# Performance work log

Hardware: AMD Instinct MI355X
Metric: run time of the kernel (lower is better)

Reference implementation:

```python
import jax, jax.numpy as jnp
import numpy as np

S_LEN, BATCH, D, HK, M, L, VOCAB = 1024, 4, 1024, 1024, 4096, 6, 32000
EPS = 1e-5


def layernorm(x, g, b):
    mu = x.mean(-1, keepdims=True)
    xc = x - mu
    var = (xc * xc).mean(-1, keepdims=True)
    return xc * jax.lax.rsqrt(var + EPS) * g + b


def block(z, wq, wk, wv, wc, g1, bb1, w1, b1, w2, b2, g2, bb2):
    # Faithful to the torch block: permute (1,0,2) at entry, never permute back.
    x = jnp.swapaxes(z, 0, 1)  # [B', S', d]
    d = x.shape[-1]
    Q = jnp.einsum('bsd,ed->bse', x, wq)
    K = jnp.einsum('bsd,ed->bse', x, wk)
    V = jnp.einsum('bsd,ed->bse', x, wv)
    # NOTE: scale is sqrt(embed_dim)=sqrt(d), not sqrt(k); no causal mask (faithful).
    scores = jnp.einsum('bse,bte->bst', Q, K) / jnp.sqrt(jnp.asarray(d, x.dtype))
    A = jax.nn.softmax(scores, axis=-1)
    ctx = jnp.einsum('bst,bte->bse', A, V)
    att = jnp.einsum('bse,de->bsd', ctx, wc) + x
    h = layernorm(att, g1, bb1)
    # NOTE: no nonlinearity in the FFN (faithful to the source).
    f = jnp.einsum('bsd,md->bsm', h, w1) + b1
    f = jnp.einsum('bsm,dm->bsd', f, w2) + b2
    return layernorm(f + h, g2, bb2)


def forward(x, word_emb, pos_emb, wq, wk, wv, wc, ln1_g, ln1_b, w1, b1, w2, b2,
            ln2_g, ln2_b, dec_w, dec_b, out_bias):
    S = x.shape[0]
    z = word_emb[x] * jnp.sqrt(jnp.asarray(D, word_emb.dtype))  # [S,B,d]
    z = jax.nn.relu(z + pos_emb[jnp.arange(S)][:, None, :])
    for i in range(L):  # small fixed layer count; shapes alternate layout so no scan
        z = block(z, wq[i], wk[i], wv[i], wc[i], ln1_g[i], ln1_b[i],
                  w1[i], b1[i], w2[i], b2[i], ln2_g[i], ln2_b[i])
    logits = jnp.einsum('sbd,vd->sbv', z, dec_w) + dec_b + out_bias
    return jax.nn.log_softmax(logits, axis=-1)


def setup_inputs() -> dict:
    key = jax.random.key(0)
    ks = jax.random.split(key, 16)
    std = jnp.float32(0.02)
    return {
        'x': jax.random.randint(ks[0], (S_LEN, BATCH), 0, VOCAB),
        'word_emb': jax.random.normal(ks[1], (VOCAB, D), jnp.float32) * std,
        'pos_emb': jax.random.normal(ks[2], (S_LEN, D), jnp.float32) * std,
        'wq': jax.random.normal(ks[3], (L, HK, D), jnp.float32) * std,
        'wk': jax.random.normal(ks[4], (L, HK, D), jnp.float32) * std,
        'wv': jax.random.normal(ks[5], (L, HK, D), jnp.float32) * std,
        'wc': jax.random.normal(ks[6], (L, D, HK), jnp.float32) * std,
        'ln1_g': jnp.ones((L, D), jnp.float32),
        'ln1_b': jnp.zeros((L, D), jnp.float32),
        'w1': jax.random.normal(ks[7], (L, M, D), jnp.float32) * std,
        'b1': jnp.zeros((L, M), jnp.float32),
        'w2': jax.random.normal(ks[8], (L, D, M), jnp.float32) * std,
        'b2': jnp.zeros((L, D), jnp.float32),
        'ln2_g': jnp.ones((L, D), jnp.float32),
        'ln2_b': jnp.zeros((L, D), jnp.float32),
        'dec_w': jax.random.normal(ks[9], (VOCAB, D), jnp.float32) * std,
        'dec_b': jnp.zeros((VOCAB,), jnp.float32),
        'out_bias': jnp.zeros((VOCAB,), jnp.float32),
    }


def reference(x, word_emb, pos_emb, wq, wk, wv, wc, ln1_g, ln1_b, w1, b1, w2, b2,
              ln2_g, ln2_b, dec_w, dec_b, out_bias):
    return forward(x, word_emb, pos_emb, wq, wk, wv, wc, ln1_g, ln1_b, w1, b1,
                   w2, b2, ln2_g, ln2_b, dec_w, dec_b, out_bias)
```

## Files before the change

### kernel.cpp

```cpp
#include <hip/hip_runtime.h>

typedef short short8 __attribute__((ext_vector_type(8)));
typedef float f32x4 __attribute__((ext_vector_type(4)));

#define DMODEL 1024
#define HKDIM 1024
#define MDIM 4096
#define NROW 4096
#define VOCAB 32000
#define NLAYER 6

#define GLOAD_LDS16(g, l)                                                      \
  __builtin_amdgcn_global_load_lds(                                            \
      (const __attribute__((address_space(1))) void*)(g),                      \
      (__attribute__((address_space(3))) void*)(l), 16, 0, 0)

__device__ __forceinline__ unsigned short f2bf(float f) {
  unsigned u = __float_as_uint(f);
  u += 0x7fffu + ((u >> 16) & 1u);
  return (unsigned short)(u >> 16);
}
__device__ __forceinline__ float bf2f(unsigned short h) {
  return __uint_as_float(((unsigned)h) << 16);
}
__device__ __forceinline__ float wave_sum(float v) {
  for (int o = 32; o; o >>= 1) v += __shfl_xor(v, o);
  return v;
}
__device__ __forceinline__ float wave_max(float v) {
  for (int o = 32; o; o >>= 1) v = fmaxf(v, __shfl_xor(v, o));
  return v;
}

__global__ __launch_bounds__(256) void k_embed(const int* __restrict__ x,
    const float* __restrict__ wemb, const float* __restrict__ pemb,
    float* __restrict__ z) {
  int r = blockIdx.x;
  int s = r >> 2;
  int tok = x[r];
  float4 a = ((const float4*)(wemb + (long)tok * DMODEL))[threadIdx.x];
  float4 p = ((const float4*)(pemb + (long)s * DMODEL))[threadIdx.x];
  float4 o;
  o.x = fmaxf(a.x * 32.0f + p.x, 0.0f);
  o.y = fmaxf(a.y * 32.0f + p.y, 0.0f);
  o.z = fmaxf(a.z * 32.0f + p.z, 0.0f);
  o.w = fmaxf(a.w * 32.0f + p.w, 0.0f);
  ((float4*)(z + (long)r * DMODEL))[threadIdx.x] = o;
}

__global__ __launch_bounds__(256) void k_permute(const float* __restrict__ zin,
    float* __restrict__ xf, unsigned short* __restrict__ xb, int A0, int A1) {
  int r = blockIdx.x;
  int a1 = r / A0, a0 = r - a1 * A0;
  float4 v = ((const float4*)(zin + (long)(a0 * A1 + a1) * DMODEL))[threadIdx.x];
  ((float4*)(xf + (long)r * DMODEL))[threadIdx.x] = v;
  ushort4 o = make_ushort4(f2bf(v.x), f2bf(v.y), f2bf(v.z), f2bf(v.w));
  ((ushort4*)(xb + (long)r * DMODEL))[threadIdx.x] = o;
}

__global__ __launch_bounds__(256) void k_cvt(const float* __restrict__ in,
    unsigned short* __restrict__ out, int n4) {
  int i = blockIdx.x * 256 + threadIdx.x;
  int stride = gridDim.x * 256;
  for (; i < n4; i += stride) {
    float4 v = ((const float4*)in)[i];
    ((ushort4*)out)[i] = make_ushort4(f2bf(v.x), f2bf(v.y), f2bf(v.z), f2bf(v.w));
  }
}

__global__ __launch_bounds__(256) void k_gemm_bt(
    const unsigned short* __restrict__ A, const unsigned short* __restrict__ B,
    float* __restrict__ Cf, unsigned short* __restrict__ Cb,
    const float* __restrict__ bias, const float* __restrict__ res,
    int M, int N, int K, int lda, int ldb, int ldc,
    long aB, long bB, long cB, float scale) {
  __shared__ unsigned short As[128 * 64];
  __shared__ unsigned short Bs[128 * 64];
  const int tid = threadIdx.x;
  const int gx = gridDim.x, gy = gridDim.y;

  int nwg = gx * gy * gridDim.z;
  int flat = blockIdx.x + gx * (blockIdx.y + gy * blockIdx.z);
  int q8 = nwg >> 3, r8 = nwg & 7;
  int xcd = flat & 7, inner = flat >> 3;
  int wg = (xcd < r8 ? xcd * (q8 + 1) : r8 * (q8 + 1) + (xcd - r8) * q8) + inner;
  int ty = wg % gy;
  int rest = wg / gy;
  int tx = rest % gx;
  int tz = rest / gx;

  const unsigned short* Ab = A + (long)tz * aB;
  const unsigned short* Bb = B + (long)tz * bB;
  const int row0 = ty * 128, col0 = tx * 128;
  const int lane = tid & 63, w = tid >> 6;
  const int wm = w >> 1, wn = w & 1;
  const int fr = lane & 15, fg = lane >> 4, fr7 = fr & 7;
  const int lrow = lane >> 3;
  const int lcol = ((lane & 7) ^ lrow) * 8;

  const unsigned short* aSrc = Ab + (long)(row0 + w * 32 + lrow) * lda + lcol;
  const unsigned short* bSrc = Bb + (long)(col0 + w * 32 + lrow) * ldb + lcol;
  unsigned short* aDst = As + w * 32 * 64;
  unsigned short* bDst = Bs + w * 32 * 64;

  f32x4 acc[4][4];
#pragma unroll
  for (int i = 0; i < 4; ++i)
#pragma unroll
    for (int j = 0; j < 4; ++j)
#pragma unroll
      for (int qq = 0; qq < 4; ++qq) acc[i][j][qq] = 0.0f;

  for (int k0 = 0; k0 < K; k0 += 64) {
#pragma unroll
    for (int i = 0; i < 4; ++i) {
      GLOAD_LDS16(aSrc + (long)i * 8 * lda + k0, aDst + i * 512);
      GLOAD_LDS16(bSrc + (long)i * 8 * ldb + k0, bDst + i * 512);
    }
    __syncthreads();
#pragma unroll
    for (int kk = 0; kk < 64; kk += 32) {
      short8 af[4], bfr[4];
#pragma unroll
      for (int i = 0; i < 4; ++i) {
        af[i] = *(const short8*)(As + (wm * 64 + i * 16 + fr) * 64 +
                                 (((kk >> 3) + fg) ^ fr7) * 8);
        bfr[i] = *(const short8*)(Bs + (wn * 64 + i * 16 + fr) * 64 +
                                  (((kk >> 3) + fg) ^ fr7) * 8);
      }
#pragma unroll
      for (int i = 0; i < 4; ++i)
#pragma unroll
        for (int j = 0; j < 4; ++j)
          acc[i][j] = __builtin_amdgcn_mfma_f32_16x16x32_bf16(af[i], bfr[j], acc[i][j], 0, 0, 0);
    }
    __syncthreads();
  }

#pragma unroll
  for (int j = 0; j < 4; ++j) {
    int col = col0 + wn * 64 + j * 16 + fr;
    float bv = bias ? bias[col] : 0.0f;
#pragma unroll
    for (int i = 0; i < 4; ++i) {
#pragma unroll
      for (int qq = 0; qq < 4; ++qq) {
        int row = row0 + wm * 64 + i * 16 + fg * 4 + qq;
        long off = cB * tz + (long)row * ldc + col;
        float v = acc[i][j][qq] * scale + bv;
        if (res) v += res[off];
        if (Cf) Cf[off] = v;
        if (Cb) Cb[off] = f2bf(v);
      }
    }
  }
}

__global__ __launch_bounds__(512, 2) void k_gemm8(
    const unsigned short* __restrict__ A, const unsigned short* __restrict__ B,
    float* __restrict__ Cf, unsigned short* __restrict__ Cb,
    const float* __restrict__ bias, int M, int N, int K,
    int lda, int ldb, int ldc) {
  __shared__ unsigned short As[2][256 * 64];
  __shared__ unsigned short Bs[2][256 * 64];
  const int tid = threadIdx.x;
  const int gx = gridDim.x, gy = gridDim.y;
  int nwg = gx * gy;
  int flat = blockIdx.x + gx * blockIdx.y;
  int q8 = nwg >> 3, r8 = nwg & 7;
  int xcd = flat & 7, inner = flat >> 3;
  int wg = (xcd < r8 ? xcd * (q8 + 1) : r8 * (q8 + 1) + (xcd - r8) * q8) + inner;
  int ty = wg % gy, tx = wg / gy;

  const int row0 = ty * 256, col0 = tx * 256;
  const int lane = tid & 63, w = tid >> 6;
  const int wm = w >> 2, wn = w & 3;
  const int fr = lane & 15, fg = lane >> 4, fr7 = fr & 7;
  const int srow = lane >> 3;
  const int scol = ((lane & 7) ^ srow) * 8;

  const unsigned short* pA = A + (size_t)(row0 + w * 32 + srow) * lda + scol;
  const unsigned short* pB = B + (size_t)(col0 + w * 32 + srow) * ldb + scol;
  unsigned short* aD0 = &As[0][w * 32 * 64];
  unsigned short* bD0 = &Bs[0][w * 32 * 64];
  unsigned short* aD1 = &As[1][w * 32 * 64];
  unsigned short* bD1 = &Bs[1][w * 32 * 64];

  auto stage = [&](int bf, int tk) {
    unsigned short* aD = bf ? aD1 : aD0;
    unsigned short* bD = bf ? bD1 : bD0;
#pragma unroll
    for (int i = 0; i < 4; ++i) {
      GLOAD_LDS16(pA + (size_t)i * 8 * lda + (size_t)tk * 64, aD + i * 512);
      GLOAD_LDS16(pB + (size_t)i * 8 * ldb + (size_t)tk * 64, bD + i * 512);
    }
  };
  auto rdA = [&](const unsigned short* lds, int i, int kq) -> short8 {
    return *(const short8*)(lds + (wm * 128 + i * 16 + fr) * 64 +
                            (((kq << 2) + fg) ^ fr7) * 8);
  };
  auto rdB = [&](const unsigned short* lds, int j, int kq) -> short8 {
    return *(const short8*)(lds + (wn * 64 + j * 16 + fr) * 64 +
                            (((kq << 2) + fg) ^ fr7) * 8);
  };

  f32x4 acc[8][4];
#pragma unroll
  for (int i = 0; i < 8; ++i)
#pragma unroll
    for (int j = 0; j < 4; ++j)
#pragma unroll
      for (int qq = 0; qq < 4; ++qq) acc[i][j][qq] = 0.0f;

  const int NT = K >> 6;

  stage(0, 0);
  __syncthreads();

  for (int t = 0; t < NT; ++t) {
    const unsigned short* aL = (t & 1) ? &As[1][0] : &As[0][0];
    const unsigned short* bL = (t & 1) ? &Bs[1][0] : &Bs[0][0];
    if (t + 1 < NT) stage((t & 1) ^ 1, t + 1);
#pragma unroll
    for (int kq = 0; kq < 2; ++kq) {
      short8 a8[8], b8[4];
#pragma unroll
      for (int i = 0; i < 8; ++i) a8[i] = rdA(aL, i, kq);
#pragma unroll
      for (int j = 0; j < 4; ++j) b8[j] = rdB(bL, j, kq);
#pragma unroll
      for (int i = 0; i < 8; ++i)
#pragma unroll
        for (int j = 0; j < 4; ++j)
          acc[i][j] = __builtin_amdgcn_mfma_f32_16x16x32_bf16(a8[i], b8[j], acc[i][j], 0, 0, 0);
    }
    __syncthreads();
  }

#pragma unroll
  for (int j = 0; j < 4; ++j) {
    int col = col0 + wn * 64 + j * 16 + fr;
    float bv = bias ? bias[col] : 0.0f;
#pragma unroll
    for (int i = 0; i < 8; ++i) {
#pragma unroll
      for (int qq = 0; qq < 4; ++qq) {
        int row = row0 + wm * 128 + i * 16 + fg * 4 + qq;
        size_t off = (size_t)row * ldc + col;
        float v = acc[i][j][qq] + bv;
        if (Cf) Cf[off] = v;
        if (Cb) Cb[off] = f2bf(v);
      }
    }
  }
}

__global__ __launch_bounds__(256) void k_ln(const float* __restrict__ X,
    const float* __restrict__ X2, const float* __restrict__ g,
    const float* __restrict__ b, float* __restrict__ outF,
    unsigned short* __restrict__ outB) {
  __shared__ float sm[4];
  int row = blockIdx.x, t = threadIdx.x;
  float4 v = ((const float4*)(X + (long)row * DMODEL))[t];
  if (X2) {
    float4 u = ((const float4*)(X2 + (long)row * DMODEL))[t];
    v.x += u.x; v.y += u.y; v.z += u.z; v.w += u.w;
  }
  float s = wave_sum(v.x + v.y + v.z + v.w);
  if ((t & 63) == 0) sm[t >> 6] = s;
  __syncthreads();
  float mean = (sm[0] + sm[1] + sm[2] + sm[3]) * (1.0f / DMODEL);
  __syncthreads();
  float4 c;
  c.x = v.x - mean; c.y = v.y - mean; c.z = v.z - mean; c.w = v.w - mean;
  float ss = wave_sum(c.x * c.x + c.y * c.y + c.z * c.z + c.w * c.w);
  if ((t & 63) == 0) sm[t >> 6] = ss;
  __syncthreads();
  float var = (sm[0] + sm[1] + sm[2] + sm[3]) * (1.0f / DMODEL);
  float rs = rsqrtf(var + 1e-5f);
  float4 gv = ((const float4*)g)[t], bv = ((const float4*)b)[t];
  float4 o;
  o.x = c.x * rs * gv.x + bv.x;
  o.y = c.y * rs * gv.y + bv.y;
  o.z = c.z * rs * gv.z + bv.z;
  o.w = c.w * rs * gv.w + bv.w;
  if (outF) ((float4*)(outF + (long)row * DMODEL))[t] = o;
  if (outB)
    ((ushort4*)(outB + (long)row * DMODEL))[t] =
        make_ushort4(f2bf(o.x), f2bf(o.y), f2bf(o.z), f2bf(o.w));
}

__global__ __launch_bounds__(256) void k_softmax(const float* __restrict__ S,
    unsigned short* __restrict__ A) {
  __shared__ float sm[4];
  int row = blockIdx.x, t = threadIdx.x;
  float4 v = ((const float4*)(S + (long)row * 1024))[t];
  float m = wave_max(fmaxf(fmaxf(v.x, v.y), fmaxf(v.z, v.w)));
  if ((t & 63) == 0) sm[t >> 6] = m;
  __syncthreads();
  m = fmaxf(fmaxf(sm[0], sm[1]), fmaxf(sm[2], sm[3]));
  __syncthreads();
  float4 e;
  e.x = __expf(v.x - m); e.y = __expf(v.y - m);
  e.z = __expf(v.z - m); e.w = __expf(v.w - m);
  float s = wave_sum(e.x + e.y + e.z + e.w);
  if ((t & 63) == 0) sm[t >> 6] = s;
  __syncthreads();
  float inv = 1.0f / (sm[0] + sm[1] + sm[2] + sm[3]);
  ((ushort4*)(A + (long)row * 1024))[t] =
      make_ushort4(f2bf(e.x * inv), f2bf(e.y * inv), f2bf(e.z * inv), f2bf(e.w * inv));
}

__global__ __launch_bounds__(256) void k_attn4(const unsigned short* __restrict__ QKV,
    unsigned short* __restrict__ C) {
  int bp = blockIdx.x;
  int w = threadIdx.x >> 6, lane = threadIdx.x & 63;
  const unsigned short* q = QKV + (long)(bp * 4 + w) * 3072;
  float s[4];
  for (int j = 0; j < 4; ++j) {
    const unsigned short* kj = QKV + (long)(bp * 4 + j) * 3072 + 1024;
    float a = 0.0f;
    for (int e = lane; e < 1024; e += 64) a += bf2f(q[e]) * bf2f(kj[e]);
    s[j] = wave_sum(a) * (1.0f / 32.0f);
  }
  float m = fmaxf(fmaxf(s[0], s[1]), fmaxf(s[2], s[3]));
  float e0 = __expf(s[0] - m), e1 = __expf(s[1] - m);
  float e2 = __expf(s[2] - m), e3 = __expf(s[3] - m);
  float inv = 1.0f / (e0 + e1 + e2 + e3);
  float a0 = e0 * inv, a1 = e1 * inv, a2 = e2 * inv, a3 = e3 * inv;
  unsigned short* c = C + (long)(bp * 4 + w) * 1024;
  const unsigned short* v0 = QKV + (long)(bp * 4 + 0) * 3072 + 2048;
  const unsigned short* v1 = QKV + (long)(bp * 4 + 1) * 3072 + 2048;
  const unsigned short* v2 = QKV + (long)(bp * 4 + 2) * 3072 + 2048;
  const unsigned short* v3 = QKV + (long)(bp * 4 + 3) * 3072 + 2048;
  for (int e = lane; e < 1024; e += 64) {
    float v = a0 * bf2f(v0[e]) + a1 * bf2f(v1[e]) + a2 * bf2f(v2[e]) + a3 * bf2f(v3[e]);
    c[e] = f2bf(v);
  }
}

__global__ __launch_bounds__(256) void k_transpose(const unsigned short* __restrict__ in,
    unsigned short* __restrict__ out, int rows, int cols, int ld_in, int ld_out,
    long inB, long outB) {
  __shared__ unsigned short tile[32][33];
  long ibase = (long)blockIdx.z * inB;
  long obase = (long)blockIdx.z * outB;
  int r0 = blockIdx.y * 32, c0 = blockIdx.x * 32;
  int tx = threadIdx.x, ty = threadIdx.y;
  for (int i = ty; i < 32; i += 8)
    tile[i][tx] = in[ibase + (long)(r0 + i) * ld_in + c0 + tx];
  __syncthreads();
  for (int i = ty; i < 32; i += 8)
    out[obase + (long)(c0 + i) * ld_out + r0 + tx] = tile[tx][i];
}

__global__ __launch_bounds__(320) void k_logsoftmax(float* __restrict__ L) {
  __shared__ float sm[5];
  int row = blockIdx.x, t = threadIdx.x;
  float* x = L + (long)row * VOCAB;
  float4 v[25];
  float m = -1e30f;
#pragma unroll
  for (int i = 0; i < 25; ++i) {
    v[i] = ((const float4*)x)[t + i * 320];
    m = fmaxf(m, fmaxf(fmaxf(v[i].x, v[i].y), fmaxf(v[i].z, v[i].w)));
  }
  m = wave_max(m);
  if ((t & 63) == 0) sm[t >> 6] = m;
  __syncthreads();
  m = fmaxf(fmaxf(fmaxf(sm[0], sm[1]), fmaxf(sm[2], sm[3])), sm[4]);
  __syncthreads();
  float s = 0.0f;
#pragma unroll
  for (int i = 0; i < 25; ++i)
    s += __expf(v[i].x - m) + __expf(v[i].y - m) + __expf(v[i].z - m) + __expf(v[i].w - m);
  s = wave_sum(s);
  if ((t & 63) == 0) sm[t >> 6] = s;
  __syncthreads();
  float l = m + __logf(sm[0] + sm[1] + sm[2] + sm[3] + sm[4]);
#pragma unroll
  for (int i = 0; i < 25; ++i) {
    float4 o = v[i];
    o.x -= l; o.y -= l; o.z -= l; o.w -= l;
    ((float4*)x)[t + i * 320] = o;
  }
}

__global__ __launch_bounds__(256) void k_addbias(const float* __restrict__ a,
    const float* __restrict__ b, float* __restrict__ o, int n) {
  int i = blockIdx.x * 256 + threadIdx.x;
  if (i < n) o[i] = a[i] + b[i];
}

extern "C" void kernel_launch(void* const* d_in, const int* in_sizes, int n_in,
                              void* d_out, int out_size, void* d_ws, size_t ws_size,
                              hipStream_t stream) {
  const int* x = (const int*)d_in[0];
  const float* wemb = (const float*)d_in[1];
  const float* pemb = (const float*)d_in[2];
  const float* wq = (const float*)d_in[3];
  const float* wk = (const float*)d_in[4];
  const float* wv = (const float*)d_in[5];
  const float* wc = (const float*)d_in[6];
  const float* ln1g = (const float*)d_in[7];
  const float* ln1b = (const float*)d_in[8];
  const float* w1 = (const float*)d_in[9];
  const float* b1 = (const float*)d_in[10];
  const float* w2 = (const float*)d_in[11];
  const float* b2 = (const float*)d_in[12];
  const float* ln2g = (const float*)d_in[13];
  const float* ln2b = (const float*)d_in[14];
  const float* decw = (const float*)d_in[15];
  const float* decb = (const float*)d_in[16];
  const float* obias = (const float*)d_in[17];
  float* out = (float*)d_out;

  char* ws = (char*)d_ws;
  size_t off = 0;
  auto alloc = [&](size_t bytes) -> char* {
    char* p = ws + off;
    off += (bytes + 255) & ~(size_t)255;
    return p;
  };
  float* z = (float*)alloc((size_t)NROW * DMODEL * 4);
  float* xf = (float*)alloc((size_t)NROW * DMODEL * 4);
  unsigned short* xb = (unsigned short*)alloc((size_t)NROW * DMODEL * 2);
  unsigned short* qkv = (unsigned short*)alloc((size_t)NROW * 3072 * 2);
  unsigned short* vt = (unsigned short*)alloc((size_t)NROW * HKDIM * 2);
  unsigned short* wbuf = (unsigned short*)alloc((size_t)MDIM * DMODEL * 2);
  float* tmp16 = (float*)alloc((size_t)NROW * 1024 * 4);
  unsigned short* am = (unsigned short*)alloc((size_t)NROW * 1024 * 2);
  unsigned short* ctx = (unsigned short*)alloc((size_t)NROW * HKDIM * 2);
  float* h = (float*)alloc((size_t)NROW * DMODEL * 4);
  unsigned short* hb = (unsigned short*)alloc((size_t)NROW * DMODEL * 2);
  unsigned short* f = (unsigned short*)alloc((size_t)NROW * MDIM * 2);
  unsigned short* dwb = (unsigned short*)alloc((size_t)VOCAB * DMODEL * 2);
  unsigned short* zb = (unsigned short*)alloc((size_t)NROW * DMODEL * 2);
  float* biasD = (float*)alloc((size_t)VOCAB * 4);
  (void)ws_size; (void)in_sizes; (void)n_in; (void)out_size;

  auto gemm = [&](const unsigned short* A, const unsigned short* B, float* Cf,
                  unsigned short* Cb, const float* bias, const float* res, int M,
                  int N, int K, int lda, int ldb, int ldc, int batch, long aB,
                  long bB, long cB, float scale) {
    dim3 g(N / 128, M / 128, batch);
    k_gemm_bt<<<g, dim3(256), 0, stream>>>(A, B, Cf, Cb, bias, res, M, N, K,
                                           lda, ldb, ldc, aB, bB, cB, scale);
  };
  auto gemm8 = [&](const unsigned short* A, const unsigned short* B, float* Cf,
                   unsigned short* Cb, const float* bias, int M, int N, int K,
                   int lda, int ldb, int ldc) {
    k_gemm8<<<dim3(N / 256, M / 256, 1), dim3(512), 0, stream>>>(
        A, B, Cf, Cb, bias, M, N, K, lda, ldb, ldc);
  };
  auto cvt = [&](const float* in, unsigned short* o, long n) {
    int n4 = (int)(n / 4);
    int grid = (n4 + 255) / 256;
    if (grid > 2048) grid = 2048;
    k_cvt<<<dim3(grid), dim3(256), 0, stream>>>(in, o, n4);
  };

  k_embed<<<NROW, 256, 0, stream>>>(x, wemb, pemb, z);

  for (int i = 0; i < NLAYER; ++i) {
    int A0 = (i % 2 == 0) ? 1024 : 4;
    int A1 = 4096 / A0;
    k_permute<<<NROW, 256, 0, stream>>>(z, xf, xb, A0, A1);

    cvt(wq + (long)i * HKDIM * DMODEL, wbuf, (long)HKDIM * DMODEL);
    cvt(wk + (long)i * HKDIM * DMODEL, wbuf + (size_t)1024 * DMODEL, (long)HKDIM * DMODEL);
    cvt(wv + (long)i * HKDIM * DMODEL, wbuf + (size_t)2048 * DMODEL, (long)HKDIM * DMODEL);
    gemm(xb, wbuf, nullptr, qkv, nullptr, nullptr, NROW, 3072, DMODEL,
         DMODEL, DMODEL, 3072, 1, 0, 0, 0, 1.0f);

    if (A0 == 1024) {
      gemm(qkv, qkv + 1024, tmp16, nullptr, nullptr, nullptr, 1024, 1024, 1024,
           3072, 3072, 1024, 4, (long)1024 * 3072, (long)1024 * 3072, 1 << 20,
           1.0f / 32.0f);
      k_softmax<<<NROW, 256, 0, stream>>>(tmp16, am);
      k_transpose<<<dim3(32, 32, 4), dim3(32, 8), 0, stream>>>(
          qkv + 2048, vt, 1024, 1024, 3072, 1024, (long)1024 * 3072, 1 << 20);
      gemm(am, vt, nullptr, ctx, nullptr, nullptr, 1024, 1024, 1024,
           1024, 1024, 1024, 4, 1 << 20, 1 << 20, 1 << 20, 1.0f);
    } else {
      k_attn4<<<1024, 256, 0, stream>>>(qkv, ctx);
    }

    cvt(wc + (long)i * DMODEL * HKDIM, wbuf, (long)DMODEL * HKDIM);
    gemm(ctx, wbuf, tmp16, nullptr, nullptr, xf, NROW, DMODEL, HKDIM,
         HKDIM, HKDIM, DMODEL, 1, 0, 0, 0, 1.0f);
    k_ln<<<NROW, 256, 0, stream>>>(tmp16, nullptr, ln1g + (long)i * DMODEL,
                                   ln1b + (long)i * DMODEL, h, hb);
    cvt(w1 + (long)i * MDIM * DMODEL, wbuf, (long)MDIM * DMODEL);
    gemm(hb, wbuf, nullptr, f, b1 + (long)i * MDIM, nullptr, NROW, MDIM, DMODEL,
         DMODEL, DMODEL, MDIM, 1, 0, 0, 0, 1.0f);
    cvt(w2 + (long)i * DMODEL * MDIM, wbuf, (long)DMODEL * MDIM);
    gemm(f, wbuf, tmp16, nullptr, b2 + (long)i * DMODEL, nullptr, NROW, DMODEL, MDIM,
         MDIM, MDIM, DMODEL, 1, 0, 0, 0, 1.0f);
    k_ln<<<NROW, 256, 0, stream>>>(tmp16, h, ln2g + (long)i * DMODEL,
                                   ln2b + (long)i * DMODEL, z, nullptr);
  }

  cvt(z, zb, (long)NROW * DMODEL);
  cvt(decw, dwb, (long)VOCAB * DMODEL);
  k_addbias<<<(VOCAB + 255) / 256, 256, 0, stream>>>(decb, obias, biasD, VOCAB);
  gemm8(zb, dwb, out, nullptr, biasD, NROW, VOCAB, DMODEL, DMODEL, DMODEL, VOCAB);
  k_logsoftmax<<<NROW, 320, 0, stream>>>(out);
}
```

Before: 2.518 ms.

## Store residuals and logits in bf16 to cut memory traffic

Removes the fp32 copies of the permuted input and the LN1 output. Residual adds now read the bf16 versions (xb, hb), and the xf and h buffers are gone. When workspace allows, the decoder GEMM writes bf16 logits with nontemporal stores, and a new log-softmax kernel reads them and writes the fp32 output. This cuts HBM traffic on the large 4096x32000 logits tensor and on the residual paths. The cost is extra rounding error in the residuals and logits.

```diff
diff --git a/kernel.cpp b/kernel.cpp
--- a/kernel.cpp
+++ b/kernel.cpp
@@ -49,11 +49,10 @@
 }
 
 __global__ __launch_bounds__(256) void k_permute(const float* __restrict__ zin,
-    float* __restrict__ xf, unsigned short* __restrict__ xb, int A0, int A1) {
+    unsigned short* __restrict__ xb, int A0, int A1) {
   int r = blockIdx.x;
   int a1 = r / A0, a0 = r - a1 * A0;
   float4 v = ((const float4*)(zin + (long)(a0 * A1 + a1) * DMODEL))[threadIdx.x];
-  ((float4*)(xf + (long)r * DMODEL))[threadIdx.x] = v;
   ushort4 o = make_ushort4(f2bf(v.x), f2bf(v.y), f2bf(v.z), f2bf(v.w));
   ((ushort4*)(xb + (long)r * DMODEL))[threadIdx.x] = o;
 }
@@ -71,7 +70,7 @@
 __global__ __launch_bounds__(256) void k_gemm_bt(
     const unsigned short* __restrict__ A, const unsigned short* __restrict__ B,
     float* __restrict__ Cf, unsigned short* __restrict__ Cb,
-    const float* __restrict__ bias, const float* __restrict__ res,
+    const float* __restrict__ bias, const unsigned short* __restrict__ resb,
     int M, int N, int K, int lda, int ldb, int ldc,
     long aB, long bB, long cB, float scale) {
   __shared__ unsigned short As[128 * 64];
@@ -148,7 +147,7 @@
         int row = row0 + wm * 64 + i * 16 + fg * 4 + qq;
         long off = cB * tz + (long)row * ldc + col;
         float v = acc[i][j][qq] * scale + bv;
-        if (res) v += res[off];
+        if (resb) v += bf2f(resb[off]);
         if (Cf) Cf[off] = v;
         if (Cb) Cb[off] = f2bf(v);
       }
@@ -248,23 +247,23 @@
         int row = row0 + wm * 128 + i * 16 + fg * 4 + qq;
         size_t off = (size_t)row * ldc + col;
         float v = acc[i][j][qq] + bv;
-        if (Cf) Cf[off] = v;
-        if (Cb) Cb[off] = f2bf(v);
+        if (Cf) __builtin_nontemporal_store(v, &Cf[off]);
+        if (Cb) __builtin_nontemporal_store(f2bf(v), &Cb[off]);
       }
     }
   }
 }
 
 __global__ __launch_bounds__(256) void k_ln(const float* __restrict__ X,
-    const float* __restrict__ X2, const float* __restrict__ g,
+    const unsigned short* __restrict__ X2b, const float* __restrict__ g,
     const float* __restrict__ b, float* __restrict__ outF,
     unsigned short* __restrict__ outB) {
   __shared__ float sm[4];
   int row = blockIdx.x, t = threadIdx.x;
   float4 v = ((const float4*)(X + (long)row * DMODEL))[t];
-  if (X2) {
-    float4 u = ((const float4*)(X2 + (long)row * DMODEL))[t];
-    v.x += u.x; v.y += u.y; v.z += u.z; v.w += u.w;
+  if (X2b) {
+    ushort4 u = ((const ushort4*)(X2b + (long)row * DMODEL))[t];
+    v.x += bf2f(u.x); v.y += bf2f(u.y); v.z += bf2f(u.z); v.w += bf2f(u.w);
   }
   float s = wave_sum(v.x + v.y + v.z + v.w);
   if ((t & 63) == 0) sm[t >> 6] = s;
@@ -352,6 +351,47 @@
   __syncthreads();
   for (int i = ty; i < 32; i += 8)
     out[obase + (long)(c0 + i) * ld_out + r0 + tx] = tile[tx][i];
+}
+
+__global__ __launch_bounds__(320) void k_logsoftmax_b(
+    const unsigned short* __restrict__ Lb, float* __restrict__ out) {
+  __shared__ float sm[5];
+  int row = blockIdx.x, t = threadIdx.x;
+  const unsigned long long* xr =
+      (const unsigned long long*)(Lb + (long)row * VOCAB);
+  float* yr = out + (long)row * VOCAB;
+  float4 v[25];
+  float m = -1e30f;
+#pragma unroll
+  for (int i = 0; i < 25; ++i) {
+    unsigned long long u = __builtin_nontemporal_load(&xr[t + i * 320]);
+    v[i].x = bf2f((unsigned short)(u & 0xffffu));
+    v[i].y = bf2f((unsigned short)((u >> 16) & 0xffffu));
+    v[i].z = bf2f((unsigned short)((u >> 32) & 0xffffu));
+    v[i].w = bf2f((unsigned short)(u >> 48));
+    m = fmaxf(m, fmaxf(fmaxf(v[i].x, v[i].y), fmaxf(v[i].z, v[i].w)));
+  }
+  m = wave_max(m);
+  if ((t & 63) == 0) sm[t >> 6] = m;
+  __syncthreads();
+  m = fmaxf(fmaxf(fmaxf(sm[0], sm[1]), fmaxf(sm[2], sm[3])), sm[4]);
+  __syncthreads();
+  float s = 0.0f;
+#pragma unroll
+  for (int i = 0; i < 25; ++i)
+    s += __expf(v[i].x - m) + __expf(v[i].y - m) + __expf(v[i].z - m) + __expf(v[i].w - m);
+  s = wave_sum(s);
+  if ((t & 63) == 0) sm[t >> 6] = s;
+  __syncthreads();
+  float l = m + __logf(sm[0] + sm[1] + sm[2] + sm[3] + sm[4]);
+#pragma unroll
+  for (int i = 0; i < 25; ++i) {
+    int idx = (t + i * 320) * 4;
+    __builtin_nontemporal_store(v[i].x - l, &yr[idx]);
+    __builtin_nontemporal_store(v[i].y - l, &yr[idx + 1]);
+    __builtin_nontemporal_store(v[i].z - l, &yr[idx + 2]);
+    __builtin_nontemporal_store(v[i].w - l, &yr[idx + 3]);
+  }
 }
 
 __global__ __launch_bounds__(320) void k_logsoftmax(float* __restrict__ L) {
@@ -423,7 +463,6 @@
     return p;
   };
   float* z = (float*)alloc((size_t)NROW * DMODEL * 4);
-  float* xf = (float*)alloc((size_t)NROW * DMODEL * 4);
   unsigned short* xb = (unsigned short*)alloc((size_t)NROW * DMODEL * 2);
   unsigned short* qkv = (unsigned short*)alloc((size_t)NROW * 3072 * 2);
   unsigned short* vt = (unsigned short*)alloc((size_t)NROW * HKDIM * 2);
@@ -431,20 +470,21 @@
   float* tmp16 = (float*)alloc((size_t)NROW * 1024 * 4);
   unsigned short* am = (unsigned short*)alloc((size_t)NROW * 1024 * 2);
   unsigned short* ctx = (unsigned short*)alloc((size_t)NROW * HKDIM * 2);
-  float* h = (float*)alloc((size_t)NROW * DMODEL * 4);
   unsigned short* hb = (unsigned short*)alloc((size_t)NROW * DMODEL * 2);
   unsigned short* f = (unsigned short*)alloc((size_t)NROW * MDIM * 2);
   unsigned short* dwb = (unsigned short*)alloc((size_t)VOCAB * DMODEL * 2);
   unsigned short* zb = (unsigned short*)alloc((size_t)NROW * DMODEL * 2);
   float* biasD = (float*)alloc((size_t)VOCAB * 4);
-  (void)ws_size; (void)in_sizes; (void)n_in; (void)out_size;
+  unsigned short* logits = (unsigned short*)alloc((size_t)NROW * VOCAB * 2);
+  const bool bfLogits = (off <= ws_size);
+  (void)in_sizes; (void)n_in; (void)out_size;
 
   auto gemm = [&](const unsigned short* A, const unsigned short* B, float* Cf,
-                  unsigned short* Cb, const float* bias, const float* res, int M,
-                  int N, int K, int lda, int ldb, int ldc, int batch, long aB,
-                  long bB, long cB, float scale) {
+                  unsigned short* Cb, const float* bias, const unsigned short* resb,
+                  int M, int N, int K, int lda, int ldb, int ldc, int batch,
+                  long aB, long bB, long cB, float scale) {
     dim3 g(N / 128, M / 128, batch);
-    k_gemm_bt<<<g, dim3(256), 0, stream>>>(A, B, Cf, Cb, bias, res, M, N, K,
+    k_gemm_bt<<<g, dim3(256), 0, stream>>>(A, B, Cf, Cb, bias, resb, M, N, K,
                                            lda, ldb, ldc, aB, bB, cB, scale);
   };
   auto gemm8 = [&](const unsigned short* A, const unsigned short* B, float* Cf,
@@ -465,7 +505,7 @@
   for (int i = 0; i < NLAYER; ++i) {
     int A0 = (i % 2 == 0) ? 1024 : 4;
     int A1 = 4096 / A0;
-    k_permute<<<NROW, 256, 0, stream>>>(z, xf, xb, A0, A1);
+    k_permute<<<NROW, 256, 0, stream>>>(z, xb, A0, A1);
 
     cvt(wq + (long)i * HKDIM * DMODEL, wbuf, (long)HKDIM * DMODEL);
     cvt(wk + (long)i * HKDIM * DMODEL, wbuf + (size_t)1024 * DMODEL, (long)HKDIM * DMODEL);
@@ -487,23 +527,28 @@
     }
 
     cvt(wc + (long)i * DMODEL * HKDIM, wbuf, (long)DMODEL * HKDIM);
-    gemm(ctx, wbuf, tmp16, nullptr, nullptr, xf, NROW, DMODEL, HKDIM,
+    gemm(ctx, wbuf, tmp16, nullptr, nullptr, xb, NROW, DMODEL, HKDIM,
          HKDIM, HKDIM, DMODEL, 1, 0, 0, 0, 1.0f);
     k_ln<<<NROW, 256, 0, stream>>>(tmp16, nullptr, ln1g + (long)i * DMODEL,
-                                   ln1b + (long)i * DMODEL, h, hb);
+                                   ln1b + (long)i * DMODEL, nullptr, hb);
     cvt(w1 + (long)i * MDIM * DMODEL, wbuf, (long)MDIM * DMODEL);
     gemm(hb, wbuf, nullptr, f, b1 + (long)i * MDIM, nullptr, NROW, MDIM, DMODEL,
          DMODEL, DMODEL, MDIM, 1, 0, 0, 0, 1.0f);
     cvt(w2 + (long)i * DMODEL * MDIM, wbuf, (long)DMODEL * MDIM);
     gemm(f, wbuf, tmp16, nullptr, b2 + (long)i * DMODEL, nullptr, NROW, DMODEL, MDIM,
          MDIM, MDIM, DMODEL, 1, 0, 0, 0, 1.0f);
-    k_ln<<<NROW, 256, 0, stream>>>(tmp16, h, ln2g + (long)i * DMODEL,
+    k_ln<<<NROW, 256, 0, stream>>>(tmp16, hb, ln2g + (long)i * DMODEL,
                                    ln2b + (long)i * DMODEL, z, nullptr);
   }
 
   cvt(z, zb, (long)NROW * DMODEL);
   cvt(decw, dwb, (long)VOCAB * DMODEL);
   k_addbias<<<(VOCAB + 255) / 256, 256, 0, stream>>>(decb, obias, biasD, VOCAB);
-  gemm8(zb, dwb, out, nullptr, biasD, NROW, VOCAB, DMODEL, DMODEL, DMODEL, VOCAB);
-  k_logsoftmax<<<NROW, 320, 0, stream>>>(out);
-}
+  if (bfLogits) {
+    gemm8(zb, dwb, nullptr, logits, biasD, NROW, VOCAB, DMODEL, DMODEL, DMODEL, VOCAB);
+    k_logsoftmax_b<<<NROW, 320, 0, stream>>>(logits, out);
+  } else {
+    gemm8(zb, dwb, out, nullptr, biasD, NROW, VOCAB, DMODEL, DMODEL, DMODEL, VOCAB);
+    k_logsoftmax<<<NROW, 320, 0, stream>>>(out);
+  }
+}
```

Measured after the change: 2.477 ms. About the same (-1.6%).
